# Kernel tuning notes

Measured on AMD Instinct MI355X. Metric: run time of the kernel, lower is better.

## Reference

```python
import jax, jax.numpy as jnp
import numpy as np

N_USERS = 500_000
N_ITEMS = 200_000
D_FEAT = 256
H = 32
N_EDGES = 2_000_000
NEG_SLOPE = 0.01


def _lin(k, out_dim, in_dim):
    return jax.random.normal(k, (out_dim, in_dim), jnp.float32) * (1.0 / np.sqrt(in_dim))


def setup_inputs() -> dict:
    key = jax.random.key(0)
    ks = jax.random.split(key, 24)
    src = jax.random.randint(ks[0], (N_EDGES,), 0, N_USERS)   # user ids
    dst = jax.random.randint(ks[1], (N_EDGES,), 0, N_ITEMS)   # product ids
    inp = {
        "user_ids": jnp.arange(N_USERS, dtype=jnp.int32),
        "product_ids": jnp.arange(N_ITEMS, dtype=jnp.int32),
        "product_features": jax.random.normal(ks[2], (N_ITEMS, D_FEAT), jnp.float32),
        "edge_rates": jnp.stack([src, dst]),      # user -> product
        "edge_rated_by": jnp.stack([dst, src]),   # product -> user (reverse)
        "user_emb": jax.random.normal(ks[3], (N_USERS, H), jnp.float32),
        "item_emb": jax.random.normal(ks[4], (N_ITEMS, H), jnp.float32),
        "feat_W": _lin(ks[5], H, D_FEAT),
        "feat_b": jnp.zeros((H,), jnp.float32),
    }
    # SAGEConv params: lin_l (neighbor, with bias), lin_r (root, no bias)
    names = ["up1", "pu1", "up2", "pu2"]  # up = user->product conv, pu = product->user conv
    for i, n in enumerate(names):
        inp[f"Wl_{n}"] = _lin(ks[6 + 3 * i], H, H)
        inp[f"bl_{n}"] = jnp.zeros((H,), jnp.float32)
        inp[f"Wr_{n}"] = _lin(ks[7 + 3 * i], H, H)
    return inp


def _sage(x_src, x_dst, edge_index, Wl, bl, Wr):
    # PyG SAGEConv, aggr='mean': lin_l(mean_j x_src[j]) + lin_r(x_dst)
    e_src, e_dst = edge_index[0], edge_index[1]
    n_dst = x_dst.shape[0]
    msg_sum = jax.ops.segment_sum(x_src[e_src], e_dst, num_segments=n_dst)
    cnt = jax.ops.segment_sum(jnp.ones_like(e_dst, dtype=x_src.dtype), e_dst, num_segments=n_dst)
    mean = msg_sum / jnp.maximum(cnt, 1.0)[:, None]
    return mean @ Wl.T + bl + x_dst @ Wr.T


def reference(user_ids, product_ids, product_features, edge_rates, edge_rated_by,
              user_emb, item_emb, feat_W, feat_b,
              Wl_up1, bl_up1, Wr_up1, Wl_pu1, bl_pu1, Wr_pu1,
              Wl_up2, bl_up2, Wr_up2, Wl_pu2, bl_pu2, Wr_pu2):
    lrelu = lambda x: jax.nn.leaky_relu(x, NEG_SLOPE)
    xu = user_emb[user_ids]                                    # [Nu, H]
    xp = item_emb[product_ids] + product_features @ feat_W.T + feat_b  # [Ni, H]

    # layer 1 (HeteroConv: each node type has exactly one incoming relation)
    p1 = lrelu(_sage(xu, xp, edge_rates, Wl_up1, bl_up1, Wr_up1))
    u1 = lrelu(_sage(xp, xu, edge_rated_by, Wl_pu1, bl_pu1, Wr_pu1))
    # layer 2
    p2 = lrelu(_sage(u1, p1, edge_rates, Wl_up2, bl_up2, Wr_up2))
    u2 = lrelu(_sage(p1, u1, edge_rated_by, Wl_pu2, bl_pu2, Wr_pu2))

    final_user = jnp.concatenate([xu, u1, u2], axis=1)   # [Nu, 3H]
    final_item = jnp.concatenate([xp, p1, p2], axis=1)   # [Ni, 3H]
    return final_user, final_item
```

## Files before the change

kernel.cpp:

```cpp
#include <hip/hip_runtime.h>

#define NU 500000
#define NI 200000
#define NN (NU + NI)
#define NE 2000000
#define HD 32
#define DF 256
#define OC 96

__device__ __forceinline__ float lrelu(float v){ return v >= 0.f ? v : 0.01f*v; }
__device__ __forceinline__ float4 f4add(float4 a, float4 b){
  return make_float4(a.x+b.x, a.y+b.y, a.z+b.z, a.w+b.w);
}

__global__ void k_zero_i32(int* __restrict__ p, int n){
  int i = blockIdx.x*blockDim.x + threadIdx.x;
  if (i < n) p[i] = 0;
}

__global__ void k_init_user(const int* __restrict__ ids, const float* __restrict__ emb,
                            float* __restrict__ outu){
  int i = blockIdx.x*blockDim.x + threadIdx.x;
  if (i >= NU) return;
  int uid = ids[i];
  const float4* s = (const float4*)(emb + (size_t)uid*HD);
  float4* d = (float4*)(outu + (size_t)i*OC);
  #pragma unroll
  for (int q = 0; q < 8; ++q) d[q] = s[q];
}

__global__ __launch_bounds__(512) void k_init_item(
    const int* __restrict__ ids, const float* __restrict__ emb,
    const float* __restrict__ feat, const float* __restrict__ W,
    const float* __restrict__ bias, float* __restrict__ outi){
  __shared__ float combo[256*34];
  int t = threadIdx.x;
  int r = t & 255;
  int seg = __builtin_amdgcn_readfirstlane(t >> 8);
  int row = blockIdx.x*256 + r;
  bool valid = row < NI;
  float acc[HD];
  #pragma unroll
  for (int h = 0; h < HD; ++h) acc[h] = 0.f;

  if (valid) {
    const float4* f4 = (const float4*)(feat + (size_t)row*DF + seg*128);
    float4 a0 = f4[0], a1 = f4[1];
    for (int k0 = 0; k0 < 128; k0 += 8) {
      float4 n0 = make_float4(0,0,0,0), n1 = n0;
      if (k0 + 8 < 128) { n0 = f4[(k0>>2)+2]; n1 = f4[(k0>>2)+3]; }
      float fv[8] = {a0.x,a0.y,a0.z,a0.w,a1.x,a1.y,a1.z,a1.w};
      #pragma unroll
      for (int kk = 0; kk < 8; ++kk) {
        #pragma unroll
        for (int h = 0; h < HD; ++h)
          acc[h] += fv[kk]*W[h*DF + seg*128 + k0 + kk];
      }
      a0 = n0; a1 = n1;
    }
  }
  if (seg == 1) {
    float2* c2 = (float2*)(combo + r*34);
    #pragma unroll
    for (int q = 0; q < 16; ++q) c2[q] = make_float2(acc[2*q], acc[2*q+1]);
  }
  __syncthreads();
  if (seg == 0 && valid) {
    const float2* c2 = (const float2*)(combo + r*34);
    #pragma unroll
    for (int q = 0; q < 16; ++q) { float2 v = c2[q]; acc[2*q] += v.x; acc[2*q+1] += v.y; }
    int pid = ids[row];
    const float4* ev = (const float4*)(emb + (size_t)pid*HD);
    const float4* bv = (const float4*)bias;
    float4* dst = (float4*)(outi + (size_t)row*OC);
    #pragma unroll
    for (int q = 0; q < 8; ++q) {
      float4 e = ev[q], b = bv[q];
      dst[q] = make_float4(acc[4*q+0]+e.x+b.x, acc[4*q+1]+e.y+b.y,
                           acc[4*q+2]+e.z+b.z, acc[4*q+3]+e.w+b.w);
    }
  }
}

__global__ void k_deg(const int* __restrict__ esrc, const int* __restrict__ edst,
                      int* __restrict__ cnt){
  int e = blockIdx.x*blockDim.x + threadIdx.x;
  if (e >= NE) return;
  atomicAdd(cnt + esrc[e], 1);
  atomicAdd(cnt + NU + edst[e], 1);
}

__global__ void k_scan1(const int* __restrict__ cnt, int* __restrict__ off,
                        int* __restrict__ part, int n){
  __shared__ int s[256];
  int t = threadIdx.x, i = blockIdx.x*256 + t;
  int v = (i < n) ? cnt[i] : 0;
  s[t] = v; __syncthreads();
  for (int o = 1; o < 256; o <<= 1) {
    int x = (t >= o) ? s[t-o] : 0;
    __syncthreads(); s[t] += x; __syncthreads();
  }
  if (i < n) off[i] = s[t] - v;
  if (t == 255) part[blockIdx.x] = s[255];
}

__global__ void k_scan2(int* __restrict__ part, int nb){
  __shared__ int s[256];
  __shared__ int carry;
  int t = threadIdx.x;
  if (t == 0) carry = 0;
  __syncthreads();
  for (int c0 = 0; c0 < nb; c0 += 256) {
    int i = c0 + t;
    int v = (i < nb) ? part[i] : 0;
    s[t] = v; __syncthreads();
    for (int o = 1; o < 256; o <<= 1) {
      int x = (t >= o) ? s[t-o] : 0;
      __syncthreads(); s[t] += x; __syncthreads();
    }
    int total = s[255];
    if (i < nb) part[i] = carry + s[t] - v;
    __syncthreads();
    if (t == 0) carry += total;
    __syncthreads();
  }
}

__global__ void k_scan3(int* __restrict__ off, const int* __restrict__ part, int n){
  int i = blockIdx.x*256 + threadIdx.x;
  if (i < n) off[i] += part[blockIdx.x];
}

__global__ void k_scatter(const int* __restrict__ esrc, const int* __restrict__ edst,
                          const int* __restrict__ off, int* __restrict__ cur,
                          int* __restrict__ nbr){
  int e = blockIdx.x*blockDim.x + threadIdx.x;
  if (e >= NE) return;
  int u = esrc[e], p = edst[e];
  int s1 = off[u]      + atomicAdd(cur + u,      1); nbr[s1] = p;
  int s2 = off[NU + p] + atomicAdd(cur + NU + p, 1); nbr[s2] = u;
}

__global__ void k_pull_fin(float* __restrict__ dstbase, int n, int nodebase,
                           const float* __restrict__ srcbase, int soff, int xoff, int outoff,
                           const int* __restrict__ off, const int* __restrict__ cnt,
                           const int* __restrict__ nbr,
                           const float* __restrict__ Wl, const float* __restrict__ bl,
                           const float* __restrict__ Wr){
  int tid = blockIdx.x*256 + threadIdx.x;
  int node = tid >> 3;
  if (node >= n) return;
  int q = tid & 7;
  int gnode = nodebase + node;
  int deg = cnt[gnode];
  int start = off[gnode];

  float4 xv = *(const float4*)(dstbase + (size_t)node*OC + xoff + q*4);

  const float* sb = srcbase + soff + q*4;
  float4 z = make_float4(0,0,0,0);
  float4 a0 = z, a1 = z, a2 = z, a3 = z;
  int j = 0;
  for (; j + 4 <= deg; j += 4) {
    int s0 = nbr[start+j+0], s1 = nbr[start+j+1];
    int s2 = nbr[start+j+2], s3 = nbr[start+j+3];
    float4 r0 = *(const float4*)(sb + (size_t)s0*OC);
    float4 r1 = *(const float4*)(sb + (size_t)s1*OC);
    float4 r2 = *(const float4*)(sb + (size_t)s2*OC);
    float4 r3 = *(const float4*)(sb + (size_t)s3*OC);
    a0 = f4add(a0, r0); a1 = f4add(a1, r1);
    a2 = f4add(a2, r2); a3 = f4add(a3, r3);
  }
  for (; j < deg; ++j) {
    int s = nbr[start+j];
    a0 = f4add(a0, *(const float4*)(sb + (size_t)s*OC));
  }
  a0 = f4add(f4add(a0, a1), f4add(a2, a3));
  float inv = 1.f / (float)(deg < 1 ? 1 : deg);
  float m0[4] = {a0.x*inv, a0.y*inv, a0.z*inv, a0.w*inv};
  float x0[4] = {xv.x, xv.y, xv.z, xv.w};

  bool b1 = (q & 1), b2 = (q & 2), b4 = (q & 4);
  float tm1[8], tx1[8];
  #pragma unroll
  for (int k = 0; k < 4; ++k) {
    float om = __shfl_xor(m0[k], 1), ox = __shfl_xor(x0[k], 1);
    tm1[k]   = b1 ? om    : m0[k];  tx1[k]   = b1 ? ox    : x0[k];
    tm1[k+4] = b1 ? m0[k] : om;     tx1[k+4] = b1 ? x0[k] : ox;
  }
  float tm2[16], tx2[16];
  #pragma unroll
  for (int k = 0; k < 8; ++k) {
    float om = __shfl_xor(tm1[k], 2), ox = __shfl_xor(tx1[k], 2);
    tm2[k]   = b2 ? om     : tm1[k];  tx2[k]   = b2 ? ox     : tx1[k];
    tm2[k+8] = b2 ? tm1[k] : om;      tx2[k+8] = b2 ? tx1[k] : ox;
  }
  float m[32], x[32];
  #pragma unroll
  for (int k = 0; k < 16; ++k) {
    float om = __shfl_xor(tm2[k], 4), ox = __shfl_xor(tx2[k], 4);
    m[k]    = b4 ? om     : tm2[k];  x[k]    = b4 ? ox     : tx2[k];
    m[k+16] = b4 ? tm2[k] : om;      x[k+16] = b4 ? tx2[k] : ox;
  }

  float y[4];
  #pragma unroll
  for (int k = 0; k < 4; ++k) {
    int h = q*4 + k;
    float s = bl[h];
    const float4* wl = (const float4*)(Wl + h*HD);
    const float4* wr = (const float4*)(Wr + h*HD);
    #pragma unroll
    for (int j4 = 0; j4 < 8; ++j4) {
      float4 wv = wl[j4];
      s += m[4*j4+0]*wv.x + m[4*j4+1]*wv.y + m[4*j4+2]*wv.z + m[4*j4+3]*wv.w;
    }
    #pragma unroll
    for (int j4 = 0; j4 < 8; ++j4) {
      float4 wv = wr[j4];
      s += x[4*j4+0]*wv.x + x[4*j4+1]*wv.y + x[4*j4+2]*wv.z + x[4*j4+3]*wv.w;
    }
    y[k] = lrelu(s);
  }
  *(float4*)(dstbase + (size_t)node*OC + outoff + q*4) = make_float4(y[0],y[1],y[2],y[3]);
}

extern "C" void kernel_launch(void* const* d_in, const int* in_sizes, int n_in,
                              void* d_out, int out_size, void* d_ws, size_t ws_size,
                              hipStream_t stream) {
  const int*   user_ids = (const int*)d_in[0];
  const int*   prod_ids = (const int*)d_in[1];
  const float* feat     = (const float*)d_in[2];
  const int*   er       = (const int*)d_in[3];
  const float* uemb     = (const float*)d_in[5];
  const float* iemb     = (const float*)d_in[6];
  const float* fW       = (const float*)d_in[7];
  const float* fb       = (const float*)d_in[8];
  const float* Wl_up1 = (const float*)d_in[9];
  const float* bl_up1 = (const float*)d_in[10];
  const float* Wr_up1 = (const float*)d_in[11];
  const float* Wl_pu1 = (const float*)d_in[12];
  const float* bl_pu1 = (const float*)d_in[13];
  const float* Wr_pu1 = (const float*)d_in[14];
  const float* Wl_up2 = (const float*)d_in[15];
  const float* bl_up2 = (const float*)d_in[16];
  const float* Wr_up2 = (const float*)d_in[17];
  const float* Wl_pu2 = (const float*)d_in[18];
  const float* bl_pu2 = (const float*)d_in[19];
  const float* Wr_pu2 = (const float*)d_in[20];

  float* outu = (float*)d_out;
  float* outi = outu + (size_t)NU*OC;

  int* cnt  = (int*)d_ws;
  int* cur  = cnt + NN;
  int* off  = cur + NN;
  int* part = off + NN;
  int* nbr  = part + 2736;

  const int* er_src = er;
  const int* er_dst = er + NE;

  const int B = 256;
  const int NB1 = (NN + 255)/256;

  k_zero_i32<<<(2*NN + B - 1)/B, B, 0, stream>>>(cnt, 2*NN);
  k_deg<<<(NE + B - 1)/B, B, 0, stream>>>(er_src, er_dst, cnt);
  k_scan1<<<NB1, B, 0, stream>>>(cnt, off, part, NN);
  k_scan2<<<1, B, 0, stream>>>(part, NB1);
  k_scan3<<<NB1, B, 0, stream>>>(off, part, NN);
  k_scatter<<<(NE + B - 1)/B, B, 0, stream>>>(er_src, er_dst, off, cur, nbr);

  k_init_user<<<(NU + B - 1)/B, B, 0, stream>>>(user_ids, uemb, outu);
  k_init_item<<<(NI + 255)/256, 512, 0, stream>>>(prod_ids, iemb, feat, fW, fb, outi);

  k_pull_fin<<<((size_t)NI*8 + B - 1)/B, B, 0, stream>>>(outi, NI, NU, outu, 0, 0, 32,
                                                 off, cnt, nbr, Wl_up1, bl_up1, Wr_up1);
  k_pull_fin<<<((size_t)NU*8 + B - 1)/B, B, 0, stream>>>(outu, NU, 0, outi, 0, 0, 32,
                                                 off, cnt, nbr, Wl_pu1, bl_pu1, Wr_pu1);
  k_pull_fin<<<((size_t)NI*8 + B - 1)/B, B, 0, stream>>>(outi, NI, NU, outu, 32, 32, 64,
                                                 off, cnt, nbr, Wl_up2, bl_up2, Wr_up2);
  k_pull_fin<<<((size_t)NU*8 + B - 1)/B, B, 0, stream>>>(outu, NU, 0, outi, 32, 32, 64,
                                                 off, cnt, nbr, Wl_pu2, bl_pu2, Wr_pu2);
}
```

Measured before the change: 1.967 ms.

## Gather neighbor features from compact bf16 tables and use nontemporal streaming accesses

The init and pull kernels now also write packed bf16 copies of the node features into side tables. The gathers in the pull kernels read 8-byte bf16 rows from these tables instead of 16-byte fp32 slices of the strided 96-wide output. The point is to halve the random-gather traffic and give denser, cache-friendlier source rows. Streaming loads and stores are also switched to nontemporal hints. The cost is extra table writes and bf16 rounding in the mean aggregation, which may hurt accuracy against the fp32 reference.

```diff
diff --git a/kernel.cpp b/kernel.cpp
--- a/kernel.cpp
+++ b/kernel.cpp
@@ -8,9 +8,17 @@
 #define DF 256
 #define OC 96
 
+typedef float        f4 __attribute__((ext_vector_type(4)));
+typedef unsigned int u2 __attribute__((ext_vector_type(2)));
+typedef unsigned int u4 __attribute__((ext_vector_type(4)));
+typedef unsigned short ushort_t;
+
 __device__ __forceinline__ float lrelu(float v){ return v >= 0.f ? v : 0.01f*v; }
-__device__ __forceinline__ float4 f4add(float4 a, float4 b){
-  return make_float4(a.x+b.x, a.y+b.y, a.z+b.z, a.w+b.w);
+
+__device__ __forceinline__ unsigned int f2bf(float f){
+  unsigned int u = __float_as_uint(f);
+  u += 0x7fffu + ((u >> 16) & 1u);
+  return u >> 16;
 }
 
 __global__ void k_zero_i32(int* __restrict__ p, int n){
@@ -19,20 +27,33 @@
 }
 
 __global__ void k_init_user(const int* __restrict__ ids, const float* __restrict__ emb,
-                            float* __restrict__ outu){
+                            float* __restrict__ outu, ushort_t* __restrict__ tbl){
   int i = blockIdx.x*blockDim.x + threadIdx.x;
   if (i >= NU) return;
   int uid = ids[i];
-  const float4* s = (const float4*)(emb + (size_t)uid*HD);
-  float4* d = (float4*)(outu + (size_t)i*OC);
-  #pragma unroll
-  for (int q = 0; q < 8; ++q) d[q] = s[q];
+  const f4* s = (const f4*)(emb + (size_t)uid*HD);
+  f4* d = (f4*)(outu + (size_t)i*OC);
+  unsigned int pk[16];
+  #pragma unroll
+  for (int q = 0; q < 8; ++q) {
+    f4 v = __builtin_nontemporal_load(s + q);
+    __builtin_nontemporal_store(v, d + q);
+    pk[2*q]   = f2bf(v.x) | (f2bf(v.y) << 16);
+    pk[2*q+1] = f2bf(v.z) | (f2bf(v.w) << 16);
+  }
+  u4* t = (u4*)(tbl + (size_t)i*HD);
+  #pragma unroll
+  for (int q = 0; q < 4; ++q) {
+    u4 v; v.x = pk[4*q]; v.y = pk[4*q+1]; v.z = pk[4*q+2]; v.w = pk[4*q+3];
+    t[q] = v;
+  }
 }
 
 __global__ __launch_bounds__(512) void k_init_item(
     const int* __restrict__ ids, const float* __restrict__ emb,
     const float* __restrict__ feat, const float* __restrict__ W,
-    const float* __restrict__ bias, float* __restrict__ outi){
+    const float* __restrict__ bias, float* __restrict__ outi,
+    ushort_t* __restrict__ tbl){
   __shared__ float combo[256*34];
   int t = threadIdx.x;
   int r = t & 255;
@@ -44,11 +65,15 @@
   for (int h = 0; h < HD; ++h) acc[h] = 0.f;
 
   if (valid) {
-    const float4* f4 = (const float4*)(feat + (size_t)row*DF + seg*128);
-    float4 a0 = f4[0], a1 = f4[1];
+    const f4* f4p = (const f4*)(feat + (size_t)row*DF + seg*128);
+    f4 a0 = __builtin_nontemporal_load(f4p);
+    f4 a1 = __builtin_nontemporal_load(f4p + 1);
     for (int k0 = 0; k0 < 128; k0 += 8) {
-      float4 n0 = make_float4(0,0,0,0), n1 = n0;
-      if (k0 + 8 < 128) { n0 = f4[(k0>>2)+2]; n1 = f4[(k0>>2)+3]; }
+      f4 n0 = {0,0,0,0}, n1 = {0,0,0,0};
+      if (k0 + 8 < 128) {
+        n0 = __builtin_nontemporal_load(f4p + (k0>>2) + 2);
+        n1 = __builtin_nontemporal_load(f4p + (k0>>2) + 3);
+      }
       float fv[8] = {a0.x,a0.y,a0.z,a0.w,a1.x,a1.y,a1.z,a1.w};
       #pragma unroll
       for (int kk = 0; kk < 8; ++kk) {
@@ -70,14 +95,25 @@
     #pragma unroll
     for (int q = 0; q < 16; ++q) { float2 v = c2[q]; acc[2*q] += v.x; acc[2*q+1] += v.y; }
     int pid = ids[row];
-    const float4* ev = (const float4*)(emb + (size_t)pid*HD);
-    const float4* bv = (const float4*)bias;
-    float4* dst = (float4*)(outi + (size_t)row*OC);
+    const f4* ev = (const f4*)(emb + (size_t)pid*HD);
+    const f4* bv = (const f4*)bias;
+    f4* dst = (f4*)(outi + (size_t)row*OC);
+    unsigned int pk[16];
     #pragma unroll
     for (int q = 0; q < 8; ++q) {
-      float4 e = ev[q], b = bv[q];
-      dst[q] = make_float4(acc[4*q+0]+e.x+b.x, acc[4*q+1]+e.y+b.y,
-                           acc[4*q+2]+e.z+b.z, acc[4*q+3]+e.w+b.w);
+      f4 e = ev[q], b = bv[q];
+      f4 o;
+      o.x = acc[4*q+0]+e.x+b.x; o.y = acc[4*q+1]+e.y+b.y;
+      o.z = acc[4*q+2]+e.z+b.z; o.w = acc[4*q+3]+e.w+b.w;
+      __builtin_nontemporal_store(o, dst + q);
+      pk[2*q]   = f2bf(o.x) | (f2bf(o.y) << 16);
+      pk[2*q+1] = f2bf(o.z) | (f2bf(o.w) << 16);
+    }
+    u4* tb = (u4*)(tbl + (size_t)row*HD);
+    #pragma unroll
+    for (int q = 0; q < 4; ++q) {
+      u4 v; v.x = pk[4*q]; v.y = pk[4*q+1]; v.z = pk[4*q+2]; v.w = pk[4*q+3];
+      tb[q] = v;
     }
   }
 }
@@ -86,8 +122,10 @@
                       int* __restrict__ cnt){
   int e = blockIdx.x*blockDim.x + threadIdx.x;
   if (e >= NE) return;
-  atomicAdd(cnt + esrc[e], 1);
-  atomicAdd(cnt + NU + edst[e], 1);
+  int u = __builtin_nontemporal_load(esrc + e);
+  int p = __builtin_nontemporal_load(edst + e);
+  atomicAdd(cnt + u, 1);
+  atomicAdd(cnt + NU + p, 1);
 }
 
 __global__ void k_scan1(const int* __restrict__ cnt, int* __restrict__ off,
@@ -136,17 +174,18 @@
                           int* __restrict__ nbr){
   int e = blockIdx.x*blockDim.x + threadIdx.x;
   if (e >= NE) return;
-  int u = esrc[e], p = edst[e];
+  int u = __builtin_nontemporal_load(esrc + e);
+  int p = __builtin_nontemporal_load(edst + e);
   int s1 = off[u]      + atomicAdd(cur + u,      1); nbr[s1] = p;
   int s2 = off[NU + p] + atomicAdd(cur + NU + p, 1); nbr[s2] = u;
 }
 
 __global__ void k_pull_fin(float* __restrict__ dstbase, int n, int nodebase,
-                           const float* __restrict__ srcbase, int soff, int xoff, int outoff,
+                           const ushort_t* __restrict__ srctbl, int xoff, int outoff,
                            const int* __restrict__ off, const int* __restrict__ cnt,
                            const int* __restrict__ nbr,
                            const float* __restrict__ Wl, const float* __restrict__ bl,
-                           const float* __restrict__ Wr){
+                           const float* __restrict__ Wr, ushort_t* __restrict__ bftbl){
   int tid = blockIdx.x*256 + threadIdx.x;
   int node = tid >> 3;
   if (node >= n) return;
@@ -155,27 +194,36 @@
   int deg = cnt[gnode];
   int start = off[gnode];
 
-  float4 xv = *(const float4*)(dstbase + (size_t)node*OC + xoff + q*4);
-
-  const float* sb = srcbase + soff + q*4;
-  float4 z = make_float4(0,0,0,0);
-  float4 a0 = z, a1 = z, a2 = z, a3 = z;
+  f4 xv = __builtin_nontemporal_load((const f4*)(dstbase + (size_t)node*OC + xoff + q*4));
+
+  const u2* sb = (const u2*)srctbl + q;
+  f4 a0 = {0,0,0,0}, a1 = a0, a2 = a0, a3 = a0;
   int j = 0;
   for (; j + 4 <= deg; j += 4) {
-    int s0 = nbr[start+j+0], s1 = nbr[start+j+1];
-    int s2 = nbr[start+j+2], s3 = nbr[start+j+3];
-    float4 r0 = *(const float4*)(sb + (size_t)s0*OC);
-    float4 r1 = *(const float4*)(sb + (size_t)s1*OC);
-    float4 r2 = *(const float4*)(sb + (size_t)s2*OC);
-    float4 r3 = *(const float4*)(sb + (size_t)s3*OC);
-    a0 = f4add(a0, r0); a1 = f4add(a1, r1);
-    a2 = f4add(a2, r2); a3 = f4add(a3, r3);
+    int s0 = __builtin_nontemporal_load(nbr + start + j + 0);
+    int s1 = __builtin_nontemporal_load(nbr + start + j + 1);
+    int s2 = __builtin_nontemporal_load(nbr + start + j + 2);
+    int s3 = __builtin_nontemporal_load(nbr + start + j + 3);
+    u2 r0 = sb[(size_t)s0*8];
+    u2 r1 = sb[(size_t)s1*8];
+    u2 r2 = sb[(size_t)s2*8];
+    u2 r3 = sb[(size_t)s3*8];
+    a0.x += __uint_as_float(r0.x << 16); a0.y += __uint_as_float(r0.x & 0xffff0000u);
+    a0.z += __uint_as_float(r0.y << 16); a0.w += __uint_as_float(r0.y & 0xffff0000u);
+    a1.x += __uint_as_float(r1.x << 16); a1.y += __uint_as_float(r1.x & 0xffff0000u);
+    a1.z += __uint_as_float(r1.y << 16); a1.w += __uint_as_float(r1.y & 0xffff0000u);
+    a2.x += __uint_as_float(r2.x << 16); a2.y += __uint_as_float(r2.x & 0xffff0000u);
+    a2.z += __uint_as_float(r2.y << 16); a2.w += __uint_as_float(r2.y & 0xffff0000u);
+    a3.x += __uint_as_float(r3.x << 16); a3.y += __uint_as_float(r3.x & 0xffff0000u);
+    a3.z += __uint_as_float(r3.y << 16); a3.w += __uint_as_float(r3.y & 0xffff0000u);
   }
   for (; j < deg; ++j) {
-    int s = nbr[start+j];
-    a0 = f4add(a0, *(const float4*)(sb + (size_t)s*OC));
-  }
-  a0 = f4add(f4add(a0, a1), f4add(a2, a3));
+    int s = __builtin_nontemporal_load(nbr + start + j);
+    u2 r = sb[(size_t)s*8];
+    a0.x += __uint_as_float(r.x << 16); a0.y += __uint_as_float(r.x & 0xffff0000u);
+    a0.z += __uint_as_float(r.y << 16); a0.w += __uint_as_float(r.y & 0xffff0000u);
+  }
+  a0 += a1 + a2 + a3;
   float inv = 1.f / (float)(deg < 1 ? 1 : deg);
   float m0[4] = {a0.x*inv, a0.y*inv, a0.z*inv, a0.w*inv};
   float x0[4] = {xv.x, xv.y, xv.z, xv.w};
@@ -208,21 +256,28 @@
   for (int k = 0; k < 4; ++k) {
     int h = q*4 + k;
     float s = bl[h];
-    const float4* wl = (const float4*)(Wl + h*HD);
-    const float4* wr = (const float4*)(Wr + h*HD);
+    const f4* wl = (const f4*)(Wl + h*HD);
+    const f4* wr = (const f4*)(Wr + h*HD);
     #pragma unroll
     for (int j4 = 0; j4 < 8; ++j4) {
-      float4 wv = wl[j4];
+      f4 wv = wl[j4];
       s += m[4*j4+0]*wv.x + m[4*j4+1]*wv.y + m[4*j4+2]*wv.z + m[4*j4+3]*wv.w;
     }
     #pragma unroll
     for (int j4 = 0; j4 < 8; ++j4) {
-      float4 wv = wr[j4];
+      f4 wv = wr[j4];
       s += x[4*j4+0]*wv.x + x[4*j4+1]*wv.y + x[4*j4+2]*wv.z + x[4*j4+3]*wv.w;
     }
     y[k] = lrelu(s);
   }
-  *(float4*)(dstbase + (size_t)node*OC + outoff + q*4) = make_float4(y[0],y[1],y[2],y[3]);
+  f4 yo; yo.x = y[0]; yo.y = y[1]; yo.z = y[2]; yo.w = y[3];
+  __builtin_nontemporal_store(yo, (f4*)(dstbase + (size_t)node*OC + outoff + q*4));
+  if (bftbl) {
+    u2 pv;
+    pv.x = f2bf(y[0]) | (f2bf(y[1]) << 16);
+    pv.y = f2bf(y[2]) | (f2bf(y[3]) << 16);
+    *((u2*)bftbl + (size_t)node*8 + q) = pv;
+  }
 }
 
 extern "C" void kernel_launch(void* const* d_in, const int* in_sizes, int n_in,
@@ -257,6 +312,9 @@
   int* off  = cur + NN;
   int* part = off + NN;
   int* nbr  = part + 2736;
+  ushort_t* tblA = (ushort_t*)(nbr + 2*NE);
+  ushort_t* tblB = tblA + (size_t)NU*HD;
+  ushort_t* tblC = tblB + (size_t)NI*HD;
 
   const int* er_src = er;
   const int* er_dst = er + NE;
@@ -271,15 +329,15 @@
   k_scan3<<<NB1, B, 0, stream>>>(off, part, NN);
   k_scatter<<<(NE + B - 1)/B, B, 0, stream>>>(er_src, er_dst, off, cur, nbr);
 
-  k_init_user<<<(NU + B - 1)/B, B, 0, stream>>>(user_ids, uemb, outu);
-  k_init_item<<<(NI + 255)/256, 512, 0, stream>>>(prod_ids, iemb, feat, fW, fb, outi);
-
-  k_pull_fin<<<((size_t)NI*8 + B - 1)/B, B, 0, stream>>>(outi, NI, NU, outu, 0, 0, 32,
-                                                 off, cnt, nbr, Wl_up1, bl_up1, Wr_up1);
-  k_pull_fin<<<((size_t)NU*8 + B - 1)/B, B, 0, stream>>>(outu, NU, 0, outi, 0, 0, 32,
-                                                 off, cnt, nbr, Wl_pu1, bl_pu1, Wr_pu1);
-  k_pull_fin<<<((size_t)NI*8 + B - 1)/B, B, 0, stream>>>(outi, NI, NU, outu, 32, 32, 64,
-                                                 off, cnt, nbr, Wl_up2, bl_up2, Wr_up2);
-  k_pull_fin<<<((size_t)NU*8 + B - 1)/B, B, 0, stream>>>(outu, NU, 0, outi, 32, 32, 64,
-                                                 off, cnt, nbr, Wl_pu2, bl_pu2, Wr_pu2);
-}
+  k_init_user<<<(NU + B - 1)/B, B, 0, stream>>>(user_ids, uemb, outu, tblA);
+  k_init_item<<<(NI + 255)/256, 512, 0, stream>>>(prod_ids, iemb, feat, fW, fb, outi, tblB);
+
+  k_pull_fin<<<((size_t)NI*8 + B - 1)/B, B, 0, stream>>>(outi, NI, NU, tblA, 0, 32,
+                                     off, cnt, nbr, Wl_up1, bl_up1, Wr_up1, tblC);
+  k_pull_fin<<<((size_t)NU*8 + B - 1)/B, B, 0, stream>>>(outu, NU, 0, tblB, 0, 32,
+                                     off, cnt, nbr, Wl_pu1, bl_pu1, Wr_pu1, tblA);
+  k_pull_fin<<<((size_t)NI*8 + B - 1)/B, B, 0, stream>>>(outi, NI, NU, tblA, 32, 64,
+                                     off, cnt, nbr, Wl_up2, bl_up2, Wr_up2, (ushort_t*)nullptr);
+  k_pull_fin<<<((size_t)NU*8 + B - 1)/B, B, 0, stream>>>(outu, NU, 0, tblC, 32, 64,
+                                     off, cnt, nbr, Wl_pu2, bl_pu2, Wr_pu2, (ushort_t*)nullptr);
+}
```

New measurement: 2.185 ms. 1.11x slower.
